# Performance work log

Hardware: AMD Instinct MI355X
Metric: run time of the kernel (lower is better)

## Reference

```python
import jax, jax.numpy as jnp
import numpy as np

D_MODEL = 1024
NUM_HEADS = 16
THETA = 10000.0
BATCH = 2
SEQ = 2048


def setup_inputs() -> dict:
    key = jax.random.key(0)
    ks = jax.random.split(key, 5)
    std = (2.0 / (D_MODEL + D_MODEL)) ** 0.5
    mk = lambda k: jax.random.truncated_normal(k, -3.0, 3.0, (D_MODEL, D_MODEL), jnp.float32) * std
    return {
        'x': jax.random.normal(ks[0], (BATCH, SEQ, D_MODEL), jnp.float32),
        'Wq': mk(ks[1]),
        'Wk': mk(ks[2]),
        'Wv': mk(ks[3]),
        'Wo': mk(ks[4]),
        'token_positions': jnp.arange(SEQ, dtype=jnp.int32),
    }


def _apply_rope(x, token_positions, theta):
    # x: (B, H, S, d_k)
    d_k = x.shape[-1]
    freq = 1.0 / theta ** (jnp.arange(0, d_k, 2, dtype=jnp.float32) / d_k)  # (d_k//2,)
    freqs = token_positions.astype(jnp.float32)[:, None] * freq[None, :]   # (S, d_k//2)
    cos, sin = jnp.cos(freqs), jnp.sin(freqs)
    x_real = x[..., 0::2]
    x_imag = x[..., 1::2]
    rot_real = x_real * cos - x_imag * sin
    rot_imag = x_real * sin + x_imag * cos
    # interleave back: (..., d_k//2, 2) -> (..., d_k)
    out = jnp.stack([rot_real, rot_imag], axis=-1)
    return out.reshape(x.shape)


def reference(x, Wq, Wk, Wv, Wo, token_positions):
    B, S, D = x.shape
    H = NUM_HEADS
    d_k = D // H

    def split_heads(t):
        return t.reshape(B, S, H, d_k).transpose(0, 2, 1, 3)  # (B, H, S, d_k)

    Q = split_heads(jnp.einsum('bsd,od->bso', x, Wq))
    K = split_heads(jnp.einsum('bsd,od->bso', x, Wk))
    V = split_heads(jnp.einsum('bsd,od->bso', x, Wv))

    Q = _apply_rope(Q, token_positions, THETA)
    K = _apply_rope(K, token_positions, THETA)

    # naive materialized attention with causal mask, faithful to source
    scores = jnp.einsum('bhqd,bhkd->bhqk', Q, K)
    causal = jnp.tril(jnp.ones((S, S), dtype=bool))  # True = attend
    scores = jnp.where(causal[None, None], scores, -jnp.inf)
    scores = scores / jnp.sqrt(jnp.asarray(d_k, scores.dtype))
    probs = jax.nn.softmax(scores, axis=-1)
    attn = jnp.einsum('bhqk,bhkd->bhqd', probs, V)  # (B, H, S, d_v)

    attn = attn.transpose(0, 2, 1, 3).reshape(B, S, D)
    return jnp.einsum('bsd,od->bso', attn, Wo)
```

## Files before the change

kernel.cpp:

```cpp
#include <hip/hip_runtime.h>
#include <hip/hip_bf16.h>
#include <math.h>

#define NUM_HEADS 16
#define DK 64
#define SEQ 2048
#define BATCHN 2
#define DM 1024
#define BS (BATCHN*SEQ)
#define LSCALE 0.18033688011112042f

typedef __bf16 bf16x8 __attribute__((ext_vector_type(8)));
typedef float floatx4 __attribute__((ext_vector_type(4)));
typedef unsigned short ushort;
typedef unsigned int uint;

__device__ __forceinline__ ushort f2bu(float f){
    union { __hip_bfloat16 h; ushort u; } cv; cv.h = __float2bfloat16(f); return cv.u;
}
__device__ __forceinline__ uint packbf(float a, float b){
    return (uint)f2bu(a) | ((uint)f2bu(b) << 16);
}

__global__ __launch_bounds__(256)
void castall(const float* __restrict__ x,  const float* __restrict__ wq,
             const float* __restrict__ wk, const float* __restrict__ wv,
             const float* __restrict__ wo, ushort* __restrict__ xb,
             ushort* __restrict__ wqkb, ushort* __restrict__ wvb,
             ushort* __restrict__ wob)
{
    int bid = blockIdx.x;
    const float* src; ushort* dst; int off;
    if (bid < 2048)      { src = x;  dst = xb;             off = bid; }
    else if (bid < 2560) { src = wq; dst = wqkb;           off = bid - 2048; }
    else if (bid < 3072) { src = wk; dst = wqkb + 1048576; off = bid - 2560; }
    else if (bid < 3584) { src = wv; dst = wvb;            off = bid - 3072; }
    else                 { src = wo; dst = wob;            off = bid - 3584; }
    int i = off*2048 + threadIdx.x*8;
    float4 a = *(const float4*)(src+i);
    float4 b = *(const float4*)(src+i+4);
    uint4 o;
    o.x = packbf(a.x, a.y);
    o.y = packbf(a.z, a.w);
    o.z = packbf(b.x, b.y);
    o.w = packbf(b.z, b.w);
    *(uint4*)(dst+i) = o;
}

__global__ __launch_bounds__(256) void ropek(const int* __restrict__ pos,
                                             float2* __restrict__ tab){
    int idx = blockIdx.x*256 + threadIdx.x;
    if (idx >= SEQ*32) return;
    int s = idx >> 5, i = idx & 31;
    float invf = expf(-0.28782313662425575f * (float)i);
    float ang = (float)pos[s] * invf;
    float sn, cs; sincosf(ang, &sn, &cs);
    tab[idx] = make_float2(cs, sn);
}

__global__ __launch_bounds__(256)
void proj_fused(const ushort* __restrict__ xb, const ushort* __restrict__ Wqkb,
                const ushort* __restrict__ Wvb, ushort* __restrict__ Qb,
                ushort* __restrict__ VTp, const float2* __restrict__ rope)
{
    __shared__ ushort As[128][40];
    __shared__ ushort Bs[128][40];

    const int bid = blockIdx.x;
    const ushort* A; const ushort* W; int row0, col0, mode;
    if (bid < 512) { A = xb;  W = Wqkb; row0 = (bid >> 4) * 128;
                     col0 = (bid & 15) * 128;  mode = 1; }
    else           { int i = bid - 512; A = Wvb; W = xb;
                     row0 = (i >> 5) * 128; col0 = (i & 31) * 128; mode = 2; }

    const int t = threadIdx.x;
    const int w = t >> 6;
    const int L = t & 63;
    const int lr = L & 15;
    const int lq = L >> 4;
    const int wrow = w * 32;

    floatx4 acc[2][8];
    #pragma unroll
    for (int i = 0; i < 2; ++i)
        #pragma unroll
        for (int j = 0; j < 8; ++j)
            acc[i][j] = (floatx4){0.f,0.f,0.f,0.f};

    const int rr = t >> 2, ko = (t & 3) * 8;

    for (int k0 = 0; k0 < DM; k0 += 32) {
        const ushort* ap = A + (size_t)(row0 + rr) * DM + k0 + ko;
        uint4 va  = *(const uint4*)ap;
        uint4 va2 = *(const uint4*)(ap + (size_t)64 * DM);
        const ushort* wp = W + (size_t)(col0 + rr) * DM + k0 + ko;
        uint4 vb  = *(const uint4*)wp;
        uint4 vb2 = *(const uint4*)(wp + (size_t)64 * DM);
        *(uint4*)&As[rr][ko]      = va;
        *(uint4*)&As[rr + 64][ko] = va2;
        *(uint4*)&Bs[rr][ko]      = vb;
        *(uint4*)&Bs[rr + 64][ko] = vb2;
        __syncthreads();

        bf16x8 aF0 = *(const bf16x8*)&As[wrow + lr][lq*8];
        bf16x8 aF1 = *(const bf16x8*)&As[wrow + 16 + lr][lq*8];
        #pragma unroll
        for (int tc = 0; tc < 8; ++tc) {
            bf16x8 bF = *(const bf16x8*)&Bs[tc*16 + lr][lq*8];
            acc[0][tc] = __builtin_amdgcn_mfma_f32_16x16x32_bf16(aF0, bF, acc[0][tc], 0, 0, 0);
            acc[1][tc] = __builtin_amdgcn_mfma_f32_16x16x32_bf16(aF1, bF, acc[1][tc], 0, 0, 0);
        }
        __syncthreads();
    }

    if (mode == 2) {
        #pragma unroll
        for (int tr = 0; tr < 2; ++tr)
            #pragma unroll
            for (int tc = 0; tc < 8; ++tc)
                #pragma unroll
                for (int r = 0; r < 4; ++r) {
                    int m = row0 + wrow + tr*16 + lq*4 + r;
                    int c = col0 + tc*16 + lr;
                    VTp[(size_t)m * BS + c] = f2bu(acc[tr][tc][r]);
                }
    } else {
        const int mat = col0 >> 10;
        const int base_hh = (col0 & 1023) >> 6;
        ushort* out = Qb + (size_t)mat * (BATCHN*NUM_HEADS*SEQ*DK);
        const float qscale = mat ? 1.f : LSCALE;
        #pragma unroll
        for (int tr = 0; tr < 2; ++tr)
            #pragma unroll
            for (int tc = 0; tc < 8; ++tc)
                #pragma unroll
                for (int r = 0; r < 4; ++r) {
                    int m = row0 + wrow + tr*16 + lq*4 + r;
                    int b = m >> 11;
                    int s = m & (SEQ - 1);
                    int dd = (tc*16 + lr) & 63;
                    int hh = base_hh + (tc >> 2);
                    float v = acc[tr][tc][r];
                    float o = __shfl_xor(v, 1, 64);
                    float2 cs = rope[s*32 + (dd >> 1)];
                    float rv = (dd & 1) ? fmaf(o, cs.y,  v * cs.x)
                                        : fmaf(-o, cs.y, v * cs.x);
                    out[((size_t)((b*NUM_HEADS + hh)*SEQ + s))*DK + dd] =
                        f2bu(rv * qscale);
                }
    }
}

__global__ __launch_bounds__(256)
void gemm_out(const ushort* __restrict__ A, const ushort* __restrict__ W,
              float* __restrict__ out)
{
    __shared__ ushort As[128][40];
    __shared__ ushort Bs[128][40];

    const int t = threadIdx.x;
    const int w = t >> 6;
    const int L = t & 63;
    const int lr = L & 15;
    const int lq = L >> 4;
    const int row0 = blockIdx.y * 128;
    const int col0 = blockIdx.x * 128;
    const int wrow = w * 32;

    floatx4 acc[2][8];
    #pragma unroll
    for (int i = 0; i < 2; ++i)
        #pragma unroll
        for (int j = 0; j < 8; ++j)
            acc[i][j] = (floatx4){0.f,0.f,0.f,0.f};

    const int rr = t >> 2, ko = (t & 3) * 8;

    for (int k0 = 0; k0 < DM; k0 += 32) {
        const ushort* ap = A + (size_t)(row0 + rr) * DM + k0 + ko;
        uint4 va  = *(const uint4*)ap;
        uint4 va2 = *(const uint4*)(ap + (size_t)64 * DM);
        const ushort* wp = W + (size_t)(col0 + rr) * DM + k0 + ko;
        uint4 vb  = *(const uint4*)wp;
        uint4 vb2 = *(const uint4*)(wp + (size_t)64 * DM);
        *(uint4*)&As[rr][ko]      = va;
        *(uint4*)&As[rr + 64][ko] = va2;
        *(uint4*)&Bs[rr][ko]      = vb;
        *(uint4*)&Bs[rr + 64][ko] = vb2;
        __syncthreads();

        bf16x8 aF0 = *(const bf16x8*)&As[wrow + lr][lq*8];
        bf16x8 aF1 = *(const bf16x8*)&As[wrow + 16 + lr][lq*8];
        #pragma unroll
        for (int tc = 0; tc < 8; ++tc) {
            bf16x8 bF = *(const bf16x8*)&Bs[tc*16 + lr][lq*8];
            acc[0][tc] = __builtin_amdgcn_mfma_f32_16x16x32_bf16(aF0, bF, acc[0][tc], 0, 0, 0);
            acc[1][tc] = __builtin_amdgcn_mfma_f32_16x16x32_bf16(aF1, bF, acc[1][tc], 0, 0, 0);
        }
        __syncthreads();
    }

    #pragma unroll
    for (int tr = 0; tr < 2; ++tr)
        #pragma unroll
        for (int tc = 0; tc < 8; ++tc)
            #pragma unroll
            for (int r = 0; r < 4; ++r) {
                int m = row0 + wrow + tr*16 + lq*4 + r;
                int c = col0 + tc*16 + lr;
                out[(size_t)m * DM + c] = acc[tr][tc][r];
            }
}

__global__ __launch_bounds__(256)
void attn_mfma(const ushort* __restrict__ Qb, const ushort* __restrict__ Kb,
               const ushort* __restrict__ VT, ushort* __restrict__ attnb,
               float* __restrict__ Opart, float* __restrict__ lpart)
{
    __shared__ ushort Ks[128][72];
    __shared__ ushort Vs[64][136];
    __shared__ ushort Ps[4][16][136];

    const int t = threadIdx.x;
    const int w = t >> 6;
    const int L = t & 63;
    const int lr = L & 15, lq = L >> 4;
    const int h  = blockIdx.y;
    const int b  = blockIdx.z;

    int qt, t0, t1, chunk = 0; bool split;
    {
        const int bx = blockIdx.x;
        if (bx < 16) { qt = bx; t0 = 0; t1 = (qt >> 1) + 1; split = false; }
        else {
            int c2 = bx - 16; qt = 16 + (c2 >> 1); chunk = c2 & 1;
            int nt = (qt >> 1) + 1, half = nt >> 1;
            t0 = chunk ? half : 0; t1 = chunk ? nt : half; split = true;
        }
    }
    const int ntfull = (qt >> 1) + 1;
    const int q0 = qt * 64;
    const int qw = q0 + w * 16;
    const int qmax = q0 + 63;
    const size_t qkbase = (size_t)(b*NUM_HEADS + h) * SEQ * DK;

    bf16x8 qF0, qF1;
    {
        const ushort* qp = Qb + qkbase + (size_t)(qw + lr) * DK + lq*8;
        qF0 = *(const bf16x8*)qp;
        qF1 = *(const bf16x8*)(qp + 32);
    }

    floatx4 O[4];
    #pragma unroll
    for (int g = 0; g < 4; ++g) O[g] = (floatx4){0.f,0.f,0.f,0.f};
    float l_lane = 0.f;

    const int kr = t >> 3, kc8 = (t & 7) * 8;
    const int vr = t >> 4, vc8 = (t & 15) * 8;
    const ushort* kp0 = Kb + qkbase + (size_t)kr * DK + kc8;
    const ushort* vp0 = VT + ((size_t)(h*DK + vr)) * BS + b*SEQ + vc8;

    for (int tile = t0; tile < t1; ++tile) {
        const int kb = tile * 128;
        __syncthreads();
        {
            #pragma unroll
            for (int c = 0; c < 4; ++c) {
                uint4 kv = *(const uint4*)(kp0 + (size_t)(kb + 32*c) * DK);
                uint4 vv = *(const uint4*)(vp0 + (size_t)(16*c) * BS + kb);
                *(uint4*)&Ks[32*c + kr][kc8] = kv;
                *(uint4*)&Vs[16*c + vr][vc8] = vv;
            }
        }
        __syncthreads();

        const int nc = min(4, ((qmax - kb) >> 5) + 1);
        const int ng = nc * 2;
        const bool lastt = (tile == ntfull - 1);
        const int lim = qw + lr - kb;

        #pragma unroll
        for (int g = 0; g < 8; ++g)
            if (g < ng) {
                floatx4 s = (floatx4){0.f,0.f,0.f,0.f};
                bf16x8 kf0 = *(const bf16x8*)&Ks[g*16 + lr][lq*8];
                bf16x8 kf1 = *(const bf16x8*)&Ks[g*16 + lr][32 + lq*8];
                s = __builtin_amdgcn_mfma_f32_16x16x32_bf16(kf0, qF0, s, 0, 0, 0);
                s = __builtin_amdgcn_mfma_f32_16x16x32_bf16(kf1, qF1, s, 0, 0, 0);
                float p0, p1, p2, p3;
                if (lastt) {
                    const int kbase = g*16 + lq*4;
                    p0 = (kbase + 0 <= lim) ? exp2f(s[0]) : 0.f;
                    p1 = (kbase + 1 <= lim) ? exp2f(s[1]) : 0.f;
                    p2 = (kbase + 2 <= lim) ? exp2f(s[2]) : 0.f;
                    p3 = (kbase + 3 <= lim) ? exp2f(s[3]) : 0.f;
                } else {
                    p0 = exp2f(s[0]); p1 = exp2f(s[1]);
                    p2 = exp2f(s[2]); p3 = exp2f(s[3]);
                }
                l_lane += (p0 + p1) + (p2 + p3);
                uint2 pk;
                pk.x = packbf(p0, p1);
                pk.y = packbf(p2, p3);
                *(uint2*)&Ps[w][lr][g*16 + lq*4] = pk;
            }
        asm volatile("s_waitcnt lgkmcnt(0)" ::: "memory");

        #pragma unroll
        for (int c = 0; c < 4; ++c)
            if (c < nc) {
                bf16x8 pF = *(const bf16x8*)&Ps[w][lr][c*32 + lq*8];
                #pragma unroll
                for (int g2 = 0; g2 < 4; ++g2) {
                    bf16x8 vf = *(const bf16x8*)&Vs[g2*16 + lr][c*32 + lq*8];
                    O[g2] = __builtin_amdgcn_mfma_f32_16x16x32_bf16(pF, vf, O[g2], 0, 0, 0);
                }
            }
    }

    l_lane += __shfl_xor(l_lane, 16, 64);
    l_lane += __shfl_xor(l_lane, 32, 64);

    if (!split) {
        #pragma unroll
        for (int r = 0; r < 4; ++r) {
            float lv = __shfl(l_lane, lq*4 + r, 64);
            float li = 1.f / lv;
            int s = qw + lq*4 + r;
            #pragma unroll
            for (int g2 = 0; g2 < 4; ++g2)
                attnb[((size_t)(b*SEQ + s))*DM + h*DK + g2*16 + lr] = f2bu(O[g2][r] * li);
        }
    } else {
        const size_t tb = (size_t)((b*NUM_HEADS + h)*16 + (qt - 16)) * 2 + chunk;
        float* Op = Opart + tb * 4096;
        #pragma unroll
        for (int r = 0; r < 4; ++r) {
            int ql = w*16 + lq*4 + r;
            #pragma unroll
            for (int g2 = 0; g2 < 4; ++g2)
                Op[ql*64 + g2*16 + lr] = O[g2][r];
        }
        if (lq == 0) lpart[tb*64 + w*16 + lr] = l_lane;
    }
}

__global__ __launch_bounds__(256)
void combine(const float* __restrict__ Opart, const float* __restrict__ lpart,
             ushort* __restrict__ attnb)
{
    int gx = blockIdx.x;
    int qti = gx & 15, bh = gx >> 4;
    int h = bh & 15, b = bh >> 4;
    int qt = 16 + qti;
    int tid = threadIdx.x;
    int row = tid >> 2, c0 = (tid & 3) * 16;
    size_t tb = (size_t)(bh*16 + qti) * 2;
    const float* O0 = Opart + tb*4096 + row*64 + c0;
    const float* O1 = O0 + 4096;
    float l = lpart[tb*64 + row] + lpart[tb*64 + 64 + row];
    float li = 1.f / l;
    int s = qt*64 + row;
    ushort* dst = attnb + ((size_t)(b*SEQ + s))*DM + h*DK + c0;
    #pragma unroll
    for (int e = 0; e < 16; e += 4) {
        float4 a = *(const float4*)(O0 + e);
        float4 c = *(const float4*)(O1 + e);
        dst[e+0] = f2bu((a.x + c.x) * li);
        dst[e+1] = f2bu((a.y + c.y) * li);
        dst[e+2] = f2bu((a.z + c.z) * li);
        dst[e+3] = f2bu((a.w + c.w) * li);
    }
}

extern "C" void kernel_launch(void* const* d_in, const int* in_sizes, int n_in,
                              void* d_out, int out_size, void* d_ws, size_t ws_size,
                              hipStream_t stream) {
    const float* x   = (const float*)d_in[0];
    const float* Wq  = (const float*)d_in[1];
    const float* Wk  = (const float*)d_in[2];
    const float* Wv  = (const float*)d_in[3];
    const float* Wo  = (const float*)d_in[4];
    const int*   pos = (const int*)d_in[5];
    float* out = (float*)d_out;

    const size_t MB = 1u << 20;
    char* ws = (char*)d_ws;
    ushort* xb    = (ushort*)(ws);
    ushort* Wqkb  = (ushort*)(ws +  8*MB);
    ushort* Wvb   = (ushort*)(ws + 12*MB);
    float*  Opart = (float*)(ws);
    float*  lpart = (float*)(ws + 17*MB);
    ushort* Qb    = (ushort*)(ws + 18*MB);
    ushort* Kb    = (ushort*)(ws + 26*MB);
    ushort* VT    = (ushort*)(ws + 34*MB);
    ushort* attnb = (ushort*)(ws + 42*MB);
    float2* ropeT = (float2*)(ws + 50*MB);
    ushort* Wob   = (ushort*)(ws + 51*MB);

    dim3 blk(256);
    castall<<<4096, blk, 0, stream>>>(x, Wq, Wk, Wv, Wo, xb, Wqkb, Wvb, Wob);
    ropek<<<SEQ*32/256, blk, 0, stream>>>(pos, ropeT);

    proj_fused<<<768, blk, 0, stream>>>(xb, Wqkb, Wvb, Qb, VT, ropeT);

    attn_mfma<<<dim3(48, NUM_HEADS, BATCHN), blk, 0, stream>>>(Qb, Kb, VT, attnb,
                                                               Opart, lpart);
    combine<<<512, blk, 0, stream>>>(Opart, lpart, attnb);

    gemm_out<<<dim3(8,32), blk, 0, stream>>>(attnb, Wob, out);
}
```

Measured before the change: 230.9 us.

## Shrink attention KV tiles to 64 and fold RoPE table into cast kernel

The attention kernel now processes 64-key tiles instead of 128-key tiles, so the causal-skip logic (nc/ng) goes away and shared memory per block drops. This should raise occupancy and cut wasted work on diagonal tiles, at the cost of more loop iterations and barriers per block. Separately, the RoPE table computation is merged into the cast kernel as extra blocks, which removes one kernel launch.

Result: faster. 224.0 us (-2.9%).

```diff
diff --git a/kernel.cpp b/kernel.cpp
--- a/kernel.cpp
+++ b/kernel.cpp
@@ -25,11 +25,21 @@
 __global__ __launch_bounds__(256)
 void castall(const float* __restrict__ x,  const float* __restrict__ wq,
              const float* __restrict__ wk, const float* __restrict__ wv,
-             const float* __restrict__ wo, ushort* __restrict__ xb,
-             ushort* __restrict__ wqkb, ushort* __restrict__ wvb,
-             ushort* __restrict__ wob)
+             const float* __restrict__ wo, const int* __restrict__ pos,
+             ushort* __restrict__ xb, ushort* __restrict__ wqkb,
+             ushort* __restrict__ wvb, ushort* __restrict__ wob,
+             float2* __restrict__ tab)
 {
     int bid = blockIdx.x;
+    if (bid >= 4096) {
+        int idx = (bid - 4096)*256 + threadIdx.x;
+        int s = idx >> 5, i = idx & 31;
+        float invf = expf(-0.28782313662425575f * (float)i);
+        float ang = (float)pos[s] * invf;
+        float sn, cs; sincosf(ang, &sn, &cs);
+        tab[idx] = make_float2(cs, sn);
+        return;
+    }
     const float* src; ushort* dst; int off;
     if (bid < 2048)      { src = x;  dst = xb;             off = bid; }
     else if (bid < 2560) { src = wq; dst = wqkb;           off = bid - 2048; }
@@ -45,17 +55,6 @@
     o.z = packbf(b.x, b.y);
     o.w = packbf(b.z, b.w);
     *(uint4*)(dst+i) = o;
-}
-
-__global__ __launch_bounds__(256) void ropek(const int* __restrict__ pos,
-                                             float2* __restrict__ tab){
-    int idx = blockIdx.x*256 + threadIdx.x;
-    if (idx >= SEQ*32) return;
-    int s = idx >> 5, i = idx & 31;
-    float invf = expf(-0.28782313662425575f * (float)i);
-    float ang = (float)pos[s] * invf;
-    float sn, cs; sincosf(ang, &sn, &cs);
-    tab[idx] = make_float2(cs, sn);
 }
 
 __global__ __launch_bounds__(256)
@@ -217,9 +216,9 @@
                const ushort* __restrict__ VT, ushort* __restrict__ attnb,
                float* __restrict__ Opart, float* __restrict__ lpart)
 {
-    __shared__ ushort Ks[128][72];
-    __shared__ ushort Vs[64][136];
-    __shared__ ushort Ps[4][16][136];
+    __shared__ ushort Ks[64][72];
+    __shared__ ushort Vs[64][72];
+    __shared__ ushort Ps[4][16][72];
 
     const int t = threadIdx.x;
     const int w = t >> 6;
@@ -231,17 +230,16 @@
     int qt, t0, t1, chunk = 0; bool split;
     {
         const int bx = blockIdx.x;
-        if (bx < 16) { qt = bx; t0 = 0; t1 = (qt >> 1) + 1; split = false; }
+        if (bx < 16) { qt = bx; t0 = 0; t1 = qt + 1; split = false; }
         else {
             int c2 = bx - 16; qt = 16 + (c2 >> 1); chunk = c2 & 1;
-            int nt = (qt >> 1) + 1, half = nt >> 1;
+            int nt = qt + 1, half = nt >> 1;
             t0 = chunk ? half : 0; t1 = chunk ? nt : half; split = true;
         }
     }
-    const int ntfull = (qt >> 1) + 1;
+    const int ntfull = qt + 1;
     const int q0 = qt * 64;
     const int qw = q0 + w * 16;
-    const int qmax = q0 + 63;
     const size_t qkbase = (size_t)(b*NUM_HEADS + h) * SEQ * DK;
 
     bf16x8 qF0, qF1;
@@ -256,67 +254,63 @@
     for (int g = 0; g < 4; ++g) O[g] = (floatx4){0.f,0.f,0.f,0.f};
     float l_lane = 0.f;
 
-    const int kr = t >> 3, kc8 = (t & 7) * 8;
-    const int vr = t >> 4, vc8 = (t & 15) * 8;
-    const ushort* kp0 = Kb + qkbase + (size_t)kr * DK + kc8;
-    const ushort* vp0 = VT + ((size_t)(h*DK + vr)) * BS + b*SEQ + vc8;
+    const int sr = t >> 3, sc = (t & 7) * 8;
+    const ushort* kp0 = Kb + qkbase + (size_t)sr * DK + sc;
+    const ushort* vp0 = VT + ((size_t)(h*DK + sr)) * BS + b*SEQ + sc;
 
     for (int tile = t0; tile < t1; ++tile) {
-        const int kb = tile * 128;
+        const int kb = tile * 64;
         __syncthreads();
         {
-            #pragma unroll
-            for (int c = 0; c < 4; ++c) {
-                uint4 kv = *(const uint4*)(kp0 + (size_t)(kb + 32*c) * DK);
-                uint4 vv = *(const uint4*)(vp0 + (size_t)(16*c) * BS + kb);
-                *(uint4*)&Ks[32*c + kr][kc8] = kv;
-                *(uint4*)&Vs[16*c + vr][vc8] = vv;
-            }
-        }
-        __syncthreads();
-
-        const int nc = min(4, ((qmax - kb) >> 5) + 1);
-        const int ng = nc * 2;
+            uint4 k0v = *(const uint4*)(kp0 + (size_t)kb * DK);
+            uint4 k1v = *(const uint4*)(kp0 + (size_t)(kb + 32) * DK);
+            uint4 v0v = *(const uint4*)(vp0 + kb);
+            uint4 v1v = *(const uint4*)(vp0 + (size_t)32 * BS + kb);
+            *(uint4*)&Ks[sr][sc]      = k0v;
+            *(uint4*)&Ks[sr + 32][sc] = k1v;
+            *(uint4*)&Vs[sr][sc]      = v0v;
+            *(uint4*)&Vs[sr + 32][sc] = v1v;
+        }
+        __syncthreads();
+
         const bool lastt = (tile == ntfull - 1);
         const int lim = qw + lr - kb;
 
         #pragma unroll
-        for (int g = 0; g < 8; ++g)
-            if (g < ng) {
-                floatx4 s = (floatx4){0.f,0.f,0.f,0.f};
-                bf16x8 kf0 = *(const bf16x8*)&Ks[g*16 + lr][lq*8];
-                bf16x8 kf1 = *(const bf16x8*)&Ks[g*16 + lr][32 + lq*8];
-                s = __builtin_amdgcn_mfma_f32_16x16x32_bf16(kf0, qF0, s, 0, 0, 0);
-                s = __builtin_amdgcn_mfma_f32_16x16x32_bf16(kf1, qF1, s, 0, 0, 0);
-                float p0, p1, p2, p3;
-                if (lastt) {
-                    const int kbase = g*16 + lq*4;
-                    p0 = (kbase + 0 <= lim) ? exp2f(s[0]) : 0.f;
-                    p1 = (kbase + 1 <= lim) ? exp2f(s[1]) : 0.f;
-                    p2 = (kbase + 2 <= lim) ? exp2f(s[2]) : 0.f;
-                    p3 = (kbase + 3 <= lim) ? exp2f(s[3]) : 0.f;
-                } else {
-                    p0 = exp2f(s[0]); p1 = exp2f(s[1]);
-                    p2 = exp2f(s[2]); p3 = exp2f(s[3]);
-                }
-                l_lane += (p0 + p1) + (p2 + p3);
-                uint2 pk;
-                pk.x = packbf(p0, p1);
-                pk.y = packbf(p2, p3);
-                *(uint2*)&Ps[w][lr][g*16 + lq*4] = pk;
+        for (int g = 0; g < 4; ++g) {
+            floatx4 s = (floatx4){0.f,0.f,0.f,0.f};
+            bf16x8 kf0 = *(const bf16x8*)&Ks[g*16 + lr][lq*8];
+            bf16x8 kf1 = *(const bf16x8*)&Ks[g*16 + lr][32 + lq*8];
+            s = __builtin_amdgcn_mfma_f32_16x16x32_bf16(kf0, qF0, s, 0, 0, 0);
+            s = __builtin_amdgcn_mfma_f32_16x16x32_bf16(kf1, qF1, s, 0, 0, 0);
+            float p0, p1, p2, p3;
+            if (lastt) {
+                const int kbase = g*16 + lq*4;
+                p0 = (kbase + 0 <= lim) ? exp2f(s[0]) : 0.f;
+                p1 = (kbase + 1 <= lim) ? exp2f(s[1]) : 0.f;
+                p2 = (kbase + 2 <= lim) ? exp2f(s[2]) : 0.f;
+                p3 = (kbase + 3 <= lim) ? exp2f(s[3]) : 0.f;
+            } else {
+                p0 = exp2f(s[0]); p1 = exp2f(s[1]);
+                p2 = exp2f(s[2]); p3 = exp2f(s[3]);
             }
+            l_lane += (p0 + p1) + (p2 + p3);
+            uint2 pk;
+            pk.x = packbf(p0, p1);
+            pk.y = packbf(p2, p3);
+            *(uint2*)&Ps[w][lr][g*16 + lq*4] = pk;
+        }
         asm volatile("s_waitcnt lgkmcnt(0)" ::: "memory");
 
         #pragma unroll
-        for (int c = 0; c < 4; ++c)
-            if (c < nc) {
-                bf16x8 pF = *(const bf16x8*)&Ps[w][lr][c*32 + lq*8];
-                #pragma unroll
-                for (int g2 = 0; g2 < 4; ++g2) {
-                    bf16x8 vf = *(const bf16x8*)&Vs[g2*16 + lr][c*32 + lq*8];
-                    O[g2] = __builtin_amdgcn_mfma_f32_16x16x32_bf16(pF, vf, O[g2], 0, 0, 0);
-                }
+        for (int c = 0; c < 2; ++c) {
+            bf16x8 pF = *(const bf16x8*)&Ps[w][lr][c*32 + lq*8];
+            #pragma unroll
+            for (int g2 = 0; g2 < 4; ++g2) {
+                bf16x8 vf = *(const bf16x8*)&Vs[g2*16 + lr][c*32 + lq*8];
+                O[g2] = __builtin_amdgcn_mfma_f32_16x16x32_bf16(pF, vf, O[g2], 0, 0, 0);
             }
+        }
     }
 
     l_lane += __shfl_xor(l_lane, 16, 64);
@@ -400,8 +394,8 @@
     ushort* Wob   = (ushort*)(ws + 51*MB);
 
     dim3 blk(256);
-    castall<<<4096, blk, 0, stream>>>(x, Wq, Wk, Wv, Wo, xb, Wqkb, Wvb, Wob);
-    ropek<<<SEQ*32/256, blk, 0, stream>>>(pos, ropeT);
+    castall<<<4352, blk, 0, stream>>>(x, Wq, Wk, Wv, Wo, pos,
+                                      xb, Wqkb, Wvb, Wob, ropeT);
 
     proj_fused<<<768, blk, 0, stream>>>(xb, Wqkb, Wvb, Qb, VT, ropeT);
 
```
